# Kernel tuning notes

Measured on AMD Instinct MI355X. Metric: run time of the kernel, lower is better.

## Reference

```python
import jax, jax.numpy as jnp
import numpy as np

B, T, C, H = 512, 1024, 64, 128


def setup_inputs() -> dict:
    key = jax.random.key(0)
    ks = jax.random.split(key, 7)
    s = 1.0 / np.sqrt(H)  # PyTorch LSTM/Linear default init U(-1/sqrt(H), 1/sqrt(H))
    u = lambda k, shape: jax.random.uniform(k, shape, jnp.float32, -s, s)
    return {
        "x": jax.random.normal(ks[0], (B, T, C), jnp.float32),
        # Per-channel stacked LSTM params; input_size=1 so W_ih is [C, 4H]
        "W_ih": u(ks[1], (C, 4 * H)),
        "W_hh": u(ks[2], (C, 4 * H, H)),
        "b_ih": u(ks[3], (C, 4 * H)),
        "b_hh": u(ks[4], (C, 4 * H)),
        # Per-channel final Linear(H, 1)
        "W_fc": u(ks[5], (C, H)),
        "b_fc": u(ks[6], (C,)),
    }


def reference(x, W_ih, W_hh, b_ih, b_hh, W_fc, b_fc):
    # x: [B, T, C]. All channels' LSTMs run as one fused vectorized scan.
    Bx, Tx, Cx = x.shape
    Hh = W_hh.shape[-1]
    b = b_ih + b_hh  # [C, 4H]
    xt = jnp.transpose(x, (1, 0, 2))  # [T, B, C]
    h0 = jnp.zeros((Bx, Cx, Hh), x.dtype)
    c0 = jnp.zeros((Bx, Cx, Hh), x.dtype)

    def step(carry, x_t):
        h, c = carry  # each [B, C, H]
        gates = (jnp.einsum('bc,cg->bcg', x_t, W_ih)
                 + jnp.einsum('bch,cgh->bcg', h, W_hh)
                 + b)  # [B, C, 4H]
        i, f, g, o = jnp.split(gates, 4, axis=-1)  # PyTorch gate order: i, f, g, o
        i = jax.nn.sigmoid(i)
        f = jax.nn.sigmoid(f)
        g = jnp.tanh(g)
        o = jax.nn.sigmoid(o)
        c = f * c + i * g
        h = o * jnp.tanh(c)
        return (h, c), None

    (h_last, _), _ = jax.lax.scan(step, (h0, c0), xt)
    # Per-channel Linear(H, 1) on the final hidden state, then squeeze -> [B, C]
    return jnp.einsum('bch,ch->bc', h_last, W_fc) + b_fc
```

## Files before the change

kernel.cpp:

```cpp
#include <hip/hip_runtime.h>


typedef _Float16 half8 __attribute__((ext_vector_type(8)));
typedef float floatx4 __attribute__((ext_vector_type(4)));

#define LOG2E 1.44269504088896340736f

__global__ __launch_bounds__(512, 2) void lstm_fused(
    const float* __restrict__ x,
    const float* __restrict__ Wih,
    const float* __restrict__ Whh,
    const float* __restrict__ bih,
    const float* __restrict__ bhh,
    const float* __restrict__ Wfc,
    const float* __restrict__ bfc,
    float* __restrict__ out)
{
    constexpr int T = 1024, C = 64, H = 128, G = 512;
    constexpr int TC = T * C;

    __shared__ _Float16 hbuf[2][8192];
    __shared__ float xstage[2][64];

    const int bid = blockIdx.x;
    const int ch  = bid & 63;
    const int b0  = (bid >> 6) << 6;

    const int tid = threadIdx.x;
    const int w   = tid >> 6;
    const int l   = tid & 63;
    const int q   = l >> 4;
    const int li  = l & 15;

    float wihr[4], bias[4];
    half8 Wf[4][4];
#pragma unroll
    for (int ct = 0; ct < 4; ++ct) {
        const float sc = (ct == 2) ? 2.0f * LOG2E : LOG2E;
        const int col = ct * H + w * 16 + li;
        wihr[ct] = Wih[ch * G + col] * sc;
        bias[ct] = (bih[ch * G + col] + bhh[ch * G + col]) * sc;
#pragma unroll
        for (int ks = 0; ks < 4; ++ks) {
            const float* wp = &Whh[((size_t)(ch * G + col)) * H + ks * 32 + q * 8];
            half8 hv;
#pragma unroll
            for (int j = 0; j < 8; ++j) hv[j] = (_Float16)(wp[j] * sc);
            Wf[ct][ks] = hv;
        }
    }

    for (int i = tid; i < 8192; i += 512) hbuf[0][i] = (_Float16)0.0f;

    const float* xrow = x + (size_t)(b0 + (tid & 63)) * TC + ch;
    if (tid < 64) xstage[0][tid] = xrow[0];

    float cst[4][4];
#pragma unroll
    for (int rt = 0; rt < 4; ++rt)
#pragma unroll
        for (int r = 0; r < 4; ++r) cst[rt][r] = 0.0f;

    const int ks_w = w >> 1;
    const int qq_w = ((w & 1) << 1) + (li >> 3);
    const int j_w  = li & 7;
    const int rxor = qq_w & 3;
    int wel[4];
#pragma unroll
    for (int r = 0; r < 4; ++r)
        wel[r] = ks_w * 512 + (qq_w * 16 + q * 4 + (r ^ rxor)) * 8 + j_w;
    const int rdoff = (q * 16 + (li ^ (q & 3))) * 8;

    __syncthreads();

    auto step = [&](const _Float16* __restrict__ rb, _Float16* __restrict__ wb,
                    const float* __restrict__ xcur, float* __restrict__ xnxt,
                    int tn) {
        float xpre;
        if (tid < 64) xpre = xrow[tn * C];

#pragma unroll
        for (int rt = 0; rt < 4; ++rt) {
            const floatx4 xq = *(const floatx4*)&xcur[rt * 16 + q * 4];

            floatx4 acc[4];
#pragma unroll
            for (int ct = 0; ct < 4; ++ct)
#pragma unroll
                for (int r = 0; r < 4; ++r)
                    acc[ct][r] = fmaf(xq[r], wihr[ct], bias[ct]);

#pragma unroll
            for (int ks = 0; ks < 4; ++ks) {
                const half8 a = *(const half8*)&rb[(rt * 4 + ks) * 512 + rdoff];
#pragma unroll
                for (int ct = 0; ct < 4; ++ct)
                    acc[ct] = __builtin_amdgcn_mfma_f32_16x16x32_f16(a, Wf[ct][ks], acc[ct], 0, 0, 0);
            }

#pragma unroll
            for (int r = 0; r < 4; ++r) {
                const float u  = __builtin_amdgcn_exp2f(-acc[0][r]);
                const float v  = __builtin_amdgcn_exp2f(-acc[1][r]);
                const float p  = __builtin_amdgcn_exp2f(acc[2][r]);
                const float wq = __builtin_amdgcn_exp2f(-acc[3][r]);
                const float Du = 1.0f + u, Dv = 1.0f + v;
                const float Dp = 1.0f + p, Dw = 1.0f + wq;
                const float A  = Du * Dv, Bq = Dp * Dw;
                const float R  = __builtin_amdgcn_rcpf(A * Bq);
                const float RA = R * Bq;
                const float RB = R * A;
                const float ig = Dv * RA;
                const float fg = Du * RA;
                const float tg = fmaf(-2.0f, Dw * RB, 1.0f);
                const float og = Dp * RB;
                const float cn = fmaf(fg, cst[rt][r], ig * tg);
                cst[rt][r] = cn;
                const float tq = __builtin_amdgcn_fmed3f(
                    cn * (2.0f * LOG2E), -29.0f, 29.0f);
                const float hq = fmaf(-2.0f,
                    __builtin_amdgcn_rcpf(1.0f + __builtin_amdgcn_exp2f(tq)), 1.0f);
                wb[rt * 2048 + wel[r]] = (_Float16)(og * hq);
            }
        }

        if (tid < 64) xnxt[tid] = xpre;
        __syncthreads();
    };

    for (int t = 0; t < T; t += 2) {
        step(hbuf[0], hbuf[1], xstage[0], xstage[1], t + 1);
        step(hbuf[1], hbuf[0], xstage[1], xstage[0], (t + 2 < T) ? t + 2 : T - 1);
    }

    if (tid < 64) {
        const int row = tid;
        const int rt = row >> 4, m = row & 15;
        float s = bfc[ch];
#pragma unroll
        for (int hh = 0; hh < H; ++hh) {
            const int ks = hh >> 5, qq = (hh & 31) >> 3, j = hh & 7;
            const int c = qq * 16 + (m ^ (qq & 3));
            s += (float)hbuf[0][(rt * 4 + ks) * 512 + c * 8 + j] * Wfc[ch * H + hh];
        }
        out[(size_t)(b0 + row) * C + ch] = s;
    }
}

extern "C" void kernel_launch(void* const* d_in, const int* in_sizes, int n_in,
                              void* d_out, int out_size, void* d_ws, size_t ws_size,
                              hipStream_t stream) {
    const float* x   = (const float*)d_in[0];
    const float* Wih = (const float*)d_in[1];
    const float* Whh = (const float*)d_in[2];
    const float* bih = (const float*)d_in[3];
    const float* bhh = (const float*)d_in[4];
    const float* Wfc = (const float*)d_in[5];
    const float* bfc = (const float*)d_in[6];
    float* out = (float*)d_out;

    lstm_fused<<<512, 512, 0, stream>>>(x, Wih, Whh, bih, bhh, Wfc, bfc, out);
}
```

Before: 6.196 ms.

## Merge two batch tiles into one 1024-thread block per channel

Each block now handles 128 batch rows as two independent 8-wave groups sharing one workgroup, launching 256 blocks of 1024 threads instead of 512 blocks of 512. The x staging for both groups is loaded together and the per-step barrier spans all 16 waves. This aims to cut block count and barrier overhead per CU, but it couples the two groups' timesteps through a single barrier, which may reduce latency hiding compared with two independently scheduled blocks. LDS and register use per CU are roughly unchanged.

```diff
diff --git a/kernel.cpp b/kernel.cpp
--- a/kernel.cpp
+++ b/kernel.cpp
@@ -6,7 +6,7 @@
 
 #define LOG2E 1.44269504088896340736f
 
-__global__ __launch_bounds__(512, 2) void lstm_fused(
+__global__ __launch_bounds__(1024, 1) void lstm_fused(
     const float* __restrict__ x,
     const float* __restrict__ Wih,
     const float* __restrict__ Whh,
@@ -19,18 +19,20 @@
     constexpr int T = 1024, C = 64, H = 128, G = 512;
     constexpr int TC = T * C;
 
-    __shared__ _Float16 hbuf[2][8192];
-    __shared__ float xstage[2][64];
+    __shared__ _Float16 hbuf[2][2][8192];
+    __shared__ float xs[2][128];
 
     const int bid = blockIdx.x;
     const int ch  = bid & 63;
-    const int b0  = (bid >> 6) << 6;
+    const int b0  = (bid >> 6) << 7;
 
-    const int tid = threadIdx.x;
-    const int w   = tid >> 6;
-    const int l   = tid & 63;
-    const int q   = l >> 4;
-    const int li  = l & 15;
+    const int tid  = threadIdx.x;
+    const int wave = tid >> 6;
+    const int g    = wave >> 3;
+    const int w    = wave & 7;
+    const int l    = tid & 63;
+    const int q    = l >> 4;
+    const int li   = l & 15;
 
     float wihr[4], bias[4];
     half8 Wf[4][4];
@@ -50,10 +52,13 @@
         }
     }
 
-    for (int i = tid; i < 8192; i += 512) hbuf[0][i] = (_Float16)0.0f;
+    {
+        const int gtid = tid & 511;
+        for (int i = gtid; i < 8192; i += 512) hbuf[g][0][i] = (_Float16)0.0f;
+    }
 
-    const float* xrow = x + (size_t)(b0 + (tid & 63)) * TC + ch;
-    if (tid < 64) xstage[0][tid] = xrow[0];
+    const float* xrow = x + (size_t)(b0 + (tid & 127)) * TC + ch;
+    if (tid < 128) xs[0][tid] = xrow[0];
 
     float cst[4][4];
 #pragma unroll
@@ -73,11 +78,14 @@
 
     __syncthreads();
 
-    auto step = [&](const _Float16* __restrict__ rb, _Float16* __restrict__ wb,
-                    const float* __restrict__ xcur, float* __restrict__ xnxt,
-                    int tn) {
+    for (int t = 0; t < T; ++t) {
+        const _Float16* __restrict__ rb = hbuf[g][t & 1];
+        _Float16* __restrict__ wb = hbuf[g][(t & 1) ^ 1];
+        const float* __restrict__ xcur = &xs[t & 1][g * 64];
+
+        const int tn = (t + 1 < T) ? t + 1 : T - 1;
         float xpre;
-        if (tid < 64) xpre = xrow[tn * C];
+        if (tid < 128) xpre = xrow[tn * C];
 
 #pragma unroll
         for (int rt = 0; rt < 4; ++rt) {
@@ -124,26 +132,22 @@
             }
         }
 
-        if (tid < 64) xnxt[tid] = xpre;
+        if (tid < 128) xs[(t + 1) & 1][tid] = xpre;
         __syncthreads();
-    };
-
-    for (int t = 0; t < T; t += 2) {
-        step(hbuf[0], hbuf[1], xstage[0], xstage[1], t + 1);
-        step(hbuf[1], hbuf[0], xstage[1], xstage[0], (t + 2 < T) ? t + 2 : T - 1);
     }
 
-    if (tid < 64) {
-        const int row = tid;
-        const int rt = row >> 4, m = row & 15;
+    if (tid < 128) {
+        const int g2 = tid >> 6;
+        const int rr = tid & 63;
+        const int rt = rr >> 4, m = rr & 15;
         float s = bfc[ch];
 #pragma unroll
         for (int hh = 0; hh < H; ++hh) {
             const int ks = hh >> 5, qq = (hh & 31) >> 3, j = hh & 7;
             const int c = qq * 16 + (m ^ (qq & 3));
-            s += (float)hbuf[0][(rt * 4 + ks) * 512 + c * 8 + j] * Wfc[ch * H + hh];
+            s += (float)hbuf[g2][0][(rt * 4 + ks) * 512 + c * 8 + j] * Wfc[ch * H + hh];
         }
-        out[(size_t)(b0 + row) * C + ch] = s;
+        out[(size_t)(b0 + tid) * C + ch] = s;
     }
 }
 
@@ -159,5 +163,5 @@
     const float* bfc = (const float*)d_in[6];
     float* out = (float*)d_out;
 
-    lstm_fused<<<512, 512, 0, stream>>>(x, Wih, Whh, bih, bhh, Wfc, bfc, out);
+    lstm_fused<<<256, 1024, 0, stream>>>(x, Wih, Whh, bih, bhh, Wfc, bfc, out);
 }
```

Measured after the change: 24.61 ms. 297% more time.
